# Optimization experiments

Hardware: AMD Instinct MI355X
Metric: run time of the kernel (lower is better)

## Reference

```python
import jax, jax.numpy as jnp
import numpy as np

NODE_CARDS = [119, 5, 12, 12, 10, 6, 6, 2, 2]
EDGE_CARDS = [5, 6, 2]
HIDDEN = 256
LAYERS = 5
N = 60000
E = 180000
G = 2048  # num graphs (fixed num_segments)
BN_EPS = 1e-5

_NODE_OFFS = np.concatenate([[0], np.cumsum(NODE_CARDS[:-1])]).astype(np.int32)
_EDGE_OFFS = np.concatenate([[0], np.cumsum(EDGE_CARDS[:-1])]).astype(np.int32)
_NODE_MAX = np.asarray(NODE_CARDS, np.int32) - 1
_EDGE_MAX = np.asarray(EDGE_CARDS, np.int32) - 1


def _cat_sum(x, table, maxs, offs):
    # x: [N, F] int; table: [sum(cards), H] -> [N, H]
    idx = jnp.clip(x, 0, maxs[None, :]) + offs[None, :]
    return table[idx].sum(axis=1)


def setup_inputs() -> dict:
    key = jax.random.key(0)
    ks = jax.random.split(key, 32)
    w = 0.0625  # ~ xavier for 256

    def nrm(k, shape, s=w):
        return jax.random.normal(k, shape, dtype=jnp.float32) * s

    inp = {
        'x': jax.random.randint(ks[0], (N, len(NODE_CARDS)), 0, 119, dtype=jnp.int32),
        'edge_index': jax.random.randint(ks[1], (2, E), 0, N, dtype=jnp.int32),
        'edge_attr': jax.random.randint(ks[2], (E, len(EDGE_CARDS)), 0, 6, dtype=jnp.int32),
        'batch': jnp.sort(jax.random.randint(ks[3], (N,), 0, G, dtype=jnp.int32)),
        # embeddings
        'node_emb': nrm(ks[4], (int(sum(NODE_CARDS)), HIDDEN), 0.1),
        'edge_emb': nrm(ks[5], (int(sum(EDGE_CARDS)), HIDDEN), 0.1),
        'vn_emb': nrm(ks[6], (1, HIDDEN), 0.1),
        # GINE conv: eps + 2-layer MLP per layer (stacked)
        'eps': jnp.zeros((LAYERS,), jnp.float32),
        'W1': nrm(ks[7], (LAYERS, HIDDEN, HIDDEN)),
        'b1': jnp.zeros((LAYERS, HIDDEN), jnp.float32),
        'W2': nrm(ks[8], (LAYERS, HIDDEN, HIDDEN)),
        'b2': jnp.zeros((LAYERS, HIDDEN), jnp.float32),
        # BatchNorm (eval mode: running stats)
        'bn_gamma': jnp.ones((LAYERS, HIDDEN), jnp.float32),
        'bn_beta': jnp.zeros((LAYERS, HIDDEN), jnp.float32),
        'bn_mean': nrm(ks[9], (LAYERS, HIDDEN), 0.02),
        'bn_var': jnp.ones((LAYERS, HIDDEN), jnp.float32),
        # virtual-node MLP per layer
        'vW1': nrm(ks[10], (LAYERS, HIDDEN, HIDDEN)),
        'vb1': jnp.zeros((LAYERS, HIDDEN), jnp.float32),
        'vW2': nrm(ks[11], (LAYERS, HIDDEN, HIDDEN)),
        'vb2': jnp.zeros((LAYERS, HIDDEN), jnp.float32),
        # head MLP (2 layers: hidden->hidden->1)
        'hW1': nrm(ks[12], (HIDDEN, HIDDEN)),
        'hb1': jnp.zeros((HIDDEN,), jnp.float32),
        'hW2': nrm(ks[13], (HIDDEN, 1)),
        'hb2': jnp.zeros((1,), jnp.float32),
    }
    return inp


def reference(x, edge_index, edge_attr, batch,
              node_emb, edge_emb, vn_emb, eps,
              W1, b1, W2, b2,
              bn_gamma, bn_beta, bn_mean, bn_var,
              vW1, vb1, vW2, vb2,
              hW1, hb1, hW2, hb2):
    node_maxs = jnp.asarray(_NODE_MAX)
    node_offs = jnp.asarray(_NODE_OFFS)
    edge_maxs = jnp.asarray(_EDGE_MAX)
    edge_offs = jnp.asarray(_EDGE_OFFS)

    h = _cat_sum(x, node_emb, node_maxs, node_offs)          # [N, H]
    ea = _cat_sum(edge_attr, edge_emb, edge_maxs, edge_offs)  # [E, H]
    src, dst = edge_index[0], edge_index[1]

    vn = jnp.broadcast_to(vn_emb[0], (G, HIDDEN))  # [G, H]

    def mean_pool(h_):
        s = jax.ops.segment_sum(h_, batch, num_segments=G)
        cnt = jax.ops.segment_sum(jnp.ones((h_.shape[0], 1), h_.dtype), batch, num_segments=G)
        return s / jnp.maximum(cnt, 1.0)

    for l in range(LAYERS):
        h = h + vn[batch]
        # GINEConv: msg = relu(x_src + edge_attr); agg scatter-add onto dst
        msg = jax.nn.relu(h[src] + ea)                        # [E, H]
        agg = jax.ops.segment_sum(msg, dst, num_segments=N)   # [N, H]
        z = (1.0 + eps[l]) * h + agg
        z = jax.nn.relu(z @ W1[l] + b1[l]) @ W2[l] + b2[l]
        # BatchNorm1d (eval, running stats)
        z = (z - bn_mean[l]) * (bn_gamma[l] / jnp.sqrt(bn_var[l] + BN_EPS)) + bn_beta[l]
        h = jax.nn.relu(z)
        # virtual-node update
        g = mean_pool(h)
        vn = vn + (jax.nn.relu(g @ vW1[l] + vb1[l]) @ vW2[l] + vb2[l])

    g = mean_pool(h)                                          # [G, H]
    logits = (jax.nn.relu(g @ hW1 + hb1) @ hW2 + hb2).reshape(-1)  # [G]
    return logits
```

## Files before the change

### kernel.cpp

```cpp
#include <hip/hip_runtime.h>

#define NN 60000
#define NE 180000
#define NG 2048
#define NL 5
#define CAP 32

typedef unsigned short u16;
typedef unsigned int u32;
typedef __bf16 bf16x8 __attribute__((ext_vector_type(8)));
typedef float f32x4 __attribute__((ext_vector_type(4)));

__device__ __forceinline__ u16 f2bf(float f) {
    u32 u = __builtin_bit_cast(u32, f);
    u += 0x7FFFu + ((u >> 16) & 1u);
    return (u16)(u >> 16);
}
__device__ __forceinline__ float bf2f(u16 s) {
    return __builtin_bit_cast(float, (u32)s << 16);
}
__device__ __forceinline__ float bflo(u32 w) {
    return __builtin_bit_cast(float, w << 16);
}
__device__ __forceinline__ float bfhi(u32 w) {
    return __builtin_bit_cast(float, w & 0xFFFF0000u);
}
__device__ __forceinline__ u32 pack2bf(float lo, float hi) {
    return (u32)f2bf(lo) | ((u32)f2bf(hi) << 16);
}
__device__ __forceinline__ void gload_lds16(const void* g, void* l) {
    __builtin_amdgcn_global_load_lds(
        (const __attribute__((address_space(1))) unsigned int*)g,
        (__attribute__((address_space(3))) unsigned int*)l, 16, 0, 0);
}
__device__ __forceinline__ int swz(int row, int col) {
    return (row << 9) + ((((col >> 3) ^ (row & 7))) << 4) + ((col & 7) << 1);
}

__constant__ int NODE_OFF[9]  = {0, 119, 124, 136, 148, 158, 164, 170, 172};
__constant__ int NODE_MAXC[9] = {118, 4, 11, 11, 9, 5, 5, 1, 1};

__global__ __launch_bounds__(256) void k_prep_weights(
    const float* __restrict__ W1, const float* __restrict__ W2,
    const float* __restrict__ vW1, const float* __restrict__ vW2,
    const float* __restrict__ hW1, u16* __restrict__ Wt)
{
    __shared__ float lt[64][65];
    int mat = blockIdx.x >> 4;
    int tile = blockIdx.x & 15;
    int tr = (tile >> 2) * 64;
    int tc = (tile & 3) * 64;
    const float* src;
    if (mat < 5)       src = W1 + (size_t)mat * 65536;
    else if (mat < 10) src = W2 + (size_t)(mat - 5) * 65536;
    else if (mat < 15) src = vW1 + (size_t)(mat - 10) * 65536;
    else if (mat < 20) src = vW2 + (size_t)(mat - 15) * 65536;
    else               src = hW1;
    int tid = threadIdx.x;
#pragma unroll
    for (int r = 0; r < 4; ++r) {
        int k = (tid >> 4) + r * 16;
        int c = (tid & 15) * 4;
        float4 v = *(const float4*)&src[(size_t)(tr + k) * 256 + tc + c];
        lt[k][c + 0] = v.x; lt[k][c + 1] = v.y;
        lt[k][c + 2] = v.z; lt[k][c + 3] = v.w;
    }
    __syncthreads();
#pragma unroll
    for (int r = 0; r < 4; ++r) {
        int n = (tid >> 4) + r * 16;
        int k = (tid & 15) * 4;
        ushort4 o;
        o.x = f2bf(lt[k + 0][n]); o.y = f2bf(lt[k + 1][n]);
        o.z = f2bf(lt[k + 2][n]); o.w = f2bf(lt[k + 3][n]);
        *(ushort4*)&Wt[(size_t)mat * 65536 + (size_t)(tc + n) * 256 + tr + k] = o;
    }
}

__global__ __launch_bounds__(256) void k_misc(
    const float* __restrict__ eemb, const int* __restrict__ batch,
    const float* __restrict__ vn_emb,
    u16* __restrict__ comb, int* __restrict__ starts,
    float* __restrict__ vn, u16* __restrict__ vnbf, float* __restrict__ gsum)
{
    int b = blockIdx.x;
    if (b < 2048) {
        int i = b * 256 + threadIdx.x;
        float v = vn_emb[i & 255];
        vn[i] = v;
        vnbf[i] = f2bf(v);
        gsum[i] = 0.f;
    } else if (b < 2108) {
        int r = b - 2048, c = threadIdx.x;
        int a0 = r / 12, a1 = (r % 12) / 2, a2 = r & 1;
        comb[r * 256 + c] = f2bf(eemb[a0 * 256 + c] + eemb[(5 + a1) * 256 + c] +
                                 eemb[(11 + a2) * 256 + c]);
    } else {
        int g = (b - 2108) * 256 + threadIdx.x;
        if (g > NG) return;
        int lo = 0, hi = NN;
        while (lo < hi) {
            int mid = (lo + hi) >> 1;
            if (batch[mid] < g) lo = mid + 1; else hi = mid;
        }
        starts[g] = lo;
    }
}

__global__ __launch_bounds__(256) void k_embed(const int* __restrict__ x,
                                               const float* __restrict__ node_emb,
                                               u16* __restrict__ hbf,
                                               int* __restrict__ deg)
{
    int i = blockIdx.x * 4 + (threadIdx.x >> 6);
    if (i >= NN) return;
    if ((threadIdx.x & 63) == 0) deg[i] = 0;
    int c = (threadIdx.x & 63) * 4;
    float4 s = make_float4(0.f, 0.f, 0.f, 0.f);
#pragma unroll
    for (int f = 0; f < 9; ++f) {
        int xv = x[i * 9 + f];
        xv = xv < 0 ? 0 : (xv > NODE_MAXC[f] ? NODE_MAXC[f] : xv);
        const float4 t = *(const float4*)&node_emb[(size_t)(NODE_OFF[f] + xv) * 256 + c];
        s.x += t.x; s.y += t.y; s.z += t.z; s.w += t.w;
    }
    ushort4 o;
    o.x = f2bf(s.x); o.y = f2bf(s.y); o.z = f2bf(s.z); o.w = f2bf(s.w);
    *(ushort4*)&hbf[(size_t)i * 256 + c] = o;
}

__global__ __launch_bounds__(256) void k_bucket(
    const int* __restrict__ src, const int* __restrict__ dst,
    const int* __restrict__ eattr, int* __restrict__ deg, u32* __restrict__ slots)
{
    int e = blockIdx.x * 256 + threadIdx.x;
    if (e >= NE) return;
    int a0 = eattr[e * 3 + 0]; a0 = a0 < 0 ? 0 : (a0 > 4 ? 4 : a0);
    int a1 = eattr[e * 3 + 1]; a1 = a1 < 0 ? 0 : (a1 > 5 ? 5 : a1);
    int a2 = eattr[e * 3 + 2]; a2 = a2 < 0 ? 0 : (a2 > 1 ? 1 : a2);
    u32 code = (u32)(a0 * 12 + a1 * 2 + a2);
    int d = dst[e];
    int p = atomicAdd(&deg[d], 1);
    if (p < CAP) slots[(size_t)d * CAP + p] = (u32)src[e] | (code << 17);
}

__global__ __launch_bounds__(256) void k_agg(
    const u16* __restrict__ hbf, const u16* __restrict__ vnbf,
    const int* __restrict__ batch, const u32* __restrict__ slots,
    const int* __restrict__ deg, const u16* __restrict__ comb,
    u16* __restrict__ Abf, const float* __restrict__ epsp)
{
    const int wid = threadIdx.x >> 6, lane = threadIdx.x & 63;
    const int half = lane >> 5, l32 = lane & 31;
    const int d = blockIdx.x * 8 + wid * 2 + half;
    const int c = l32 * 8;
    int nd = deg[d];
    nd = nd > CAP ? CAP : nd;

    const u32* sl = slots + (size_t)d * CAP;
    u32 sv_l = (l32 < nd) ? sl[l32] : 0u;
    int b_l = (l32 < nd) ? batch[sv_l & 0x1FFFFu] : 0;

    float acc[8] = {0.f, 0.f, 0.f, 0.f, 0.f, 0.f, 0.f, 0.f};
    for (int p = 0; p < nd; ++p) {
        int srcl = (lane & 32) | p;
        u32 sv = (u32)__shfl((int)sv_l, srcl);
        int b  = __shfl(b_l, srcl);
        int s  = (int)(sv & 0x1FFFFu);
        int code = (int)(sv >> 17);
        const uint4 hv = *(const uint4*)&hbf[(size_t)s * 256 + c];
        const uint4 vv = *(const uint4*)&vnbf[(size_t)b * 256 + c];
        const uint4 tv = *(const uint4*)&comb[(size_t)code * 256 + c];
        const u32* hw = (const u32*)&hv;
        const u32* vw = (const u32*)&vv;
        const u32* tw = (const u32*)&tv;
#pragma unroll
        for (int e = 0; e < 4; ++e) {
            acc[e * 2 + 0] += fmaxf(bflo(hw[e]) + bflo(vw[e]) + bflo(tw[e]), 0.f);
            acc[e * 2 + 1] += fmaxf(bfhi(hw[e]) + bfhi(vw[e]) + bfhi(tw[e]), 0.f);
        }
    }

    int bd = batch[d];
    float ep = 1.0f + *epsp;
    const uint4 hd = *(const uint4*)&hbf[(size_t)d * 256 + c];
    const uint4 vd = *(const uint4*)&vnbf[(size_t)bd * 256 + c];
    const u32* hw = (const u32*)&hd;
    const u32* vw = (const u32*)&vd;
    uint4 o;
    u32* op = (u32*)&o;
#pragma unroll
    for (int e = 0; e < 4; ++e) {
        float lo = (bflo(hw[e]) + bflo(vw[e])) * ep + acc[e * 2 + 0];
        float hi = (bfhi(hw[e]) + bfhi(vw[e])) * ep + acc[e * 2 + 1];
        op[e] = pack2bf(lo, hi);
    }
    *(uint4*)&Abf[(size_t)d * 256 + c] = o;
}

__device__ __forceinline__ void stageW(const u16* __restrict__ W, u16* Bl,
                                       int k0, int tid, int wid)
{
#pragma unroll
    for (int i = 0; i < 4; ++i) {
        int slot = i * 512 + tid;
        int row = slot >> 3, cch = slot & 7;
        int g = cch ^ (row & 7);
        gload_lds16((const char*)W + (size_t)row * 512 + (size_t)k0 * 2 + (g << 4),
                    (char*)Bl + ((i * 512 + wid * 64) << 4));
    }
}

__device__ __forceinline__ void gemm64(const u16* Tl, u16* Bl, const u16* __restrict__ W,
                                       f32x4 (&acc)[2][4], int wm, int wn,
                                       int lane, int tid, int wid)
{
    const int cl = lane & 15;
    for (int k0 = 0; k0 < 256; k0 += 64) {
        __syncthreads();
        stageW(W, Bl, k0, tid, wid);
        __syncthreads();
#pragma unroll
        for (int kw = 0; kw < 2; ++kw) {
            int q = kw * 4 + (lane >> 4);
            int qt = (k0 >> 3) + q;
            bf16x8 af[2], bfr[4];
#pragma unroll
            for (int t = 0; t < 2; ++t) {
                int ar = wm + t * 16 + cl;
                af[t] = __builtin_bit_cast(bf16x8,
                    *(const uint4*)((const char*)Tl + (ar << 9) + ((qt ^ (ar & 7)) << 4)));
            }
#pragma unroll
            for (int t = 0; t < 4; ++t) {
                int br = wn + t * 16 + cl;
                bfr[t] = __builtin_bit_cast(bf16x8,
                    *(const uint4*)((const char*)Bl + (br << 7) + ((q ^ (br & 7)) << 4)));
            }
#pragma unroll
            for (int i = 0; i < 2; ++i)
#pragma unroll
                for (int j = 0; j < 4; ++j)
                    acc[i][j] = __builtin_amdgcn_mfma_f32_16x16x32_bf16(af[i], bfr[j], acc[i][j], 0, 0, 0);
        }
    }
}

__device__ __forceinline__ void writeT(u16* Tl, const f32x4 (&acc)[2][4],
                                       const float* __restrict__ b1,
                                       int wm, int wn, int lane)
{
    const int cl = lane & 15, rg = lane >> 4;
#pragma unroll
    for (int j = 0; j < 4; ++j) {
        int col = wn + j * 16 + cl;
        float bv = b1[col];
#pragma unroll
        for (int i = 0; i < 2; ++i)
#pragma unroll
            for (int r = 0; r < 4; ++r) {
                int row = wm + i * 16 + rg * 4 + r;
                float v = fmaxf(acc[i][j][r] + bv, 0.f);
                *(u16*)((char*)Tl + swz(row, col)) = f2bf(v);
            }
    }
}

__global__ __launch_bounds__(512) void k_mlpP(
    const u16* __restrict__ Abf, u16* __restrict__ hnxt,
    const int* __restrict__ batch,
    const u16* __restrict__ W1t, const u16* __restrict__ W2t,
    const float* __restrict__ b1, const float* __restrict__ b2,
    const float* __restrict__ bng, const float* __restrict__ bnb,
    const float* __restrict__ bnm, const float* __restrict__ bnv,
    float* __restrict__ gsum)
{
    __shared__ __align__(16) u16 Bl[256 * 64];
    __shared__ __align__(16) u16 Tl[64 * 256];
    __shared__ int batchLds[64];
    const int m0 = blockIdx.x * 64;
    const int tid = threadIdx.x, lane = tid & 63, wid = tid >> 6;
    const int wm = (wid >> 2) * 32, wn = (wid & 3) * 64;
    const int cl = lane & 15, rg = lane >> 4;

    if (tid < 64) batchLds[tid] = (m0 + tid < NN) ? batch[m0 + tid] : -1;

#pragma unroll
    for (int i = 0; i < 4; ++i) {
        int slot = i * 512 + tid;
        int row = slot >> 5, cch = slot & 31;
        int g = cch ^ (row & 7);
        gload_lds16((const char*)Abf + (size_t)(m0 + row) * 512 + (g << 4),
                    (char*)Tl + ((i * 512 + wid * 64) << 4));
    }

    f32x4 acc1[2][4] = {};
    gemm64(Tl, Bl, W1t, acc1, wm, wn, lane, tid, wid);
    __syncthreads();
    writeT(Tl, acc1, b1, wm, wn, lane);

    f32x4 acc2[2][4] = {};
    gemm64(Tl, Bl, W2t, acc2, wm, wn, lane, tid, wid);
    __syncthreads();

#pragma unroll
    for (int j = 0; j < 4; ++j) {
        int gn = wn + j * 16 + cl;
        float bv = b2[gn];
        float sc = bng[gn] * rsqrtf(bnv[gn] + 1e-5f);
        float sh = bnb[gn] - bnm[gn] * sc;
        float s = 0.f;
        int gcur = -1;
#pragma unroll
        for (int i = 0; i < 2; ++i) {
#pragma unroll
            for (int r = 0; r < 4; ++r) {
                int row = wm + i * 16 + rg * 4 + r;
                int g = batchLds[row];
                float v = acc2[i][j][r] + bv;
                u16 hb = f2bf(fmaxf(v * sc + sh, 0.f));
                if (g >= 0) hnxt[(size_t)(m0 + row) * 256 + gn] = hb;
                if (g != gcur) {
                    if (gcur >= 0) atomicAdd(&gsum[(size_t)gcur * 256 + gn], s);
                    gcur = g; s = 0.f;
                }
                if (g >= 0) s += bf2f(hb);
            }
        }
        if (gcur >= 0) atomicAdd(&gsum[(size_t)gcur * 256 + gn], s);
    }
}

__global__ __launch_bounds__(512) void k_mlpR(
    const u16* __restrict__ Abf, u16* __restrict__ hnxt,
    const int* __restrict__ batch,
    const u16* __restrict__ W1t, const u16* __restrict__ W2t,
    const float* __restrict__ b1, const float* __restrict__ b2,
    const float* __restrict__ bng, const float* __restrict__ bnb,
    const float* __restrict__ bnm, const float* __restrict__ bnv,
    float* __restrict__ gsum)
{
    __shared__ __align__(16) u16 Wl[256 * 256];
    __shared__ __align__(16) u16 Tl[64 * 256];
    const int m0 = blockIdx.x * 64;
    const int tid = threadIdx.x, lane = tid & 63, wid = tid >> 6;
    const int wm = (wid >> 2) * 32, wn = (wid & 3) * 64;
    const int cl = lane & 15, rg = lane >> 4;

#pragma unroll
    for (int i = 0; i < 4; ++i) {
        int slot = i * 512 + tid;
        int row = slot >> 5, cch = slot & 31;
        int g = cch ^ (row & 7);
        gload_lds16((const char*)Abf + (size_t)(m0 + row) * 512 + (g << 4),
                    (char*)Tl + ((i * 512 + wid * 64) << 4));
    }
#pragma unroll
    for (int i = 0; i < 16; ++i) {
        int slot = i * 512 + tid;
        int row = slot >> 5, cch = slot & 31;
        int g = cch ^ (row & 7);
        gload_lds16((const char*)W1t + (size_t)row * 512 + (g << 4),
                    (char*)Wl + ((i * 512 + wid * 64) << 4));
    }
    __syncthreads();

    f32x4 acc1[2][4] = {};
#pragma unroll
    for (int p = 0; p < 8; ++p) {
        int ch = p * 4 + rg;
        bf16x8 af[2], bfr[4];
#pragma unroll
        for (int t = 0; t < 2; ++t) {
            int ar = wm + t * 16 + cl;
            af[t] = __builtin_bit_cast(bf16x8,
                *(const uint4*)((const char*)Tl + (ar << 9) + ((ch ^ (ar & 7)) << 4)));
        }
#pragma unroll
        for (int u = 0; u < 4; ++u) {
            int br = wn + u * 16 + cl;
            bfr[u] = __builtin_bit_cast(bf16x8,
                *(const uint4*)((const char*)Wl + (br << 9) + ((ch ^ (br & 7)) << 4)));
        }
#pragma unroll
        for (int t = 0; t < 2; ++t)
#pragma unroll
            for (int u = 0; u < 4; ++u)
                acc1[t][u] = __builtin_amdgcn_mfma_f32_16x16x32_bf16(af[t], bfr[u], acc1[t][u], 0, 0, 0);
    }
    __syncthreads();

    writeT(Tl, acc1, b1, wm, wn, lane);
#pragma unroll
    for (int i = 0; i < 16; ++i) {
        int slot = i * 512 + tid;
        int row = slot >> 5, cch = slot & 31;
        int g = cch ^ (row & 7);
        gload_lds16((const char*)W2t + (size_t)row * 512 + (g << 4),
                    (char*)Wl + ((i * 512 + wid * 64) << 4));
    }
    __syncthreads();

    f32x4 acc2[2][4] = {};
#pragma unroll
    for (int p = 0; p < 8; ++p) {
        int ch = p * 4 + rg;
        bf16x8 af[2], bfr[4];
#pragma unroll
        for (int t = 0; t < 2; ++t) {
            int ar = wm + t * 16 + cl;
            af[t] = __builtin_bit_cast(bf16x8,
                *(const uint4*)((const char*)Tl + (ar << 9) + ((ch ^ (ar & 7)) << 4)));
        }
#pragma unroll
        for (int u = 0; u < 4; ++u) {
            int br = wn + u * 16 + cl;
            bfr[u] = __builtin_bit_cast(bf16x8,
                *(const uint4*)((const char*)Wl + (br << 9) + ((ch ^ (br & 7)) << 4)));
        }
#pragma unroll
        for (int t = 0; t < 2; ++t)
#pragma unroll
            for (int u = 0; u < 4; ++u)
                acc2[t][u] = __builtin_amdgcn_mfma_f32_16x16x32_bf16(af[t], bfr[u], acc2[t][u], 0, 0, 0);
    }

#pragma unroll
    for (int j = 0; j < 4; ++j) {
        int gn = wn + j * 16 + cl;
        float bv = b2[gn];
        float sc = bng[gn] * rsqrtf(bnv[gn] + 1e-5f);
        float sh = bnb[gn] - bnm[gn] * sc;
        float s = 0.f;
        int gcur = -1;
#pragma unroll
        for (int i = 0; i < 2; ++i) {
#pragma unroll
            for (int r = 0; r < 4; ++r) {
                int row = wm + i * 16 + rg * 4 + r;
                int g = (m0 + row < NN) ? batch[m0 + row] : -1;
                float v = acc2[i][j][r] + bv;
                u16 hb = f2bf(fmaxf(v * sc + sh, 0.f));
                if (g >= 0) hnxt[(size_t)(m0 + row) * 256 + gn] = hb;
                if (g != gcur) {
                    if (gcur >= 0) atomicAdd(&gsum[(size_t)gcur * 256 + gn], s);
                    gcur = g; s = 0.f;
                }
                if (g >= 0) s += bf2f(hb);
            }
        }
        if (gcur >= 0) atomicAdd(&gsum[(size_t)gcur * 256 + gn], s);
    }
}

__global__ __launch_bounds__(512) void k_vnmlp(
    float* __restrict__ gsum, const int* __restrict__ starts,
    const u16* __restrict__ W1t, const u16* __restrict__ W2t,
    const float* __restrict__ b1, const float* __restrict__ b2,
    float* __restrict__ vn, u16* __restrict__ vnbf)
{
    __shared__ __align__(16) u16 Bl[256 * 64];
    __shared__ __align__(16) u16 Tl[64 * 256];
    const int m0 = blockIdx.x * 64;
    const int tid = threadIdx.x, lane = tid & 63, wid = tid >> 6;
    const int wm = (wid >> 2) * 32, wn = (wid & 3) * 64;
    const int cl = lane & 15, rg = lane >> 4;

    {
        const int c = lane * 4;
#pragma unroll
        for (int n = 0; n < 8; ++n) {
            int row = wid * 8 + n;
            int g = m0 + row;
            float4 sv = *(const float4*)&gsum[(size_t)g * 256 + c];
            *(float4*)&gsum[(size_t)g * 256 + c] = make_float4(0.f, 0.f, 0.f, 0.f);
            float cnt = (float)(starts[g + 1] - starts[g]);
            float inv = 1.0f / fmaxf(cnt, 1.0f);
            ushort4 o;
            o.x = f2bf(sv.x * inv); o.y = f2bf(sv.y * inv);
            o.z = f2bf(sv.z * inv); o.w = f2bf(sv.w * inv);
            *(ushort4*)((char*)Tl + swz(row, c)) = o;
        }
    }
    __syncthreads();

    f32x4 acc1[2][4] = {};
    gemm64(Tl, Bl, W1t, acc1, wm, wn, lane, tid, wid);
    __syncthreads();
    writeT(Tl, acc1, b1, wm, wn, lane);

    f32x4 acc2[2][4] = {};
    gemm64(Tl, Bl, W2t, acc2, wm, wn, lane, tid, wid);

#pragma unroll
    for (int j = 0; j < 4; ++j) {
        int gn = wn + j * 16 + cl;
        float bv = b2[gn];
#pragma unroll
        for (int i = 0; i < 2; ++i) {
#pragma unroll
            for (int r = 0; r < 4; ++r) {
                int gm = m0 + wm + i * 16 + rg * 4 + r;
                size_t idx = (size_t)gm * 256 + gn;
                float nv = vn[idx] + acc2[i][j][r] + bv;
                vn[idx] = nv;
                vnbf[idx] = f2bf(nv);
            }
        }
    }
}

__global__ __launch_bounds__(512) void k_headf(
    const float* __restrict__ gsum, const int* __restrict__ starts,
    const u16* __restrict__ W1t, const float* __restrict__ b1,
    const float* __restrict__ hW2, const float* __restrict__ hb2,
    float* __restrict__ out)
{
    __shared__ __align__(16) u16 Bl[256 * 64];
    __shared__ __align__(16) u16 Tl[64 * 256];
    const int m0 = blockIdx.x * 64;
    const int tid = threadIdx.x, lane = tid & 63, wid = tid >> 6;
    const int wm = (wid >> 2) * 32, wn = (wid & 3) * 64;

    {
        const int c = lane * 4;
#pragma unroll
        for (int n = 0; n < 8; ++n) {
            int row = wid * 8 + n;
            int g = m0 + row;
            float4 sv = *(const float4*)&gsum[(size_t)g * 256 + c];
            float cnt = (float)(starts[g + 1] - starts[g]);
            float inv = 1.0f / fmaxf(cnt, 1.0f);
            ushort4 o;
            o.x = f2bf(sv.x * inv); o.y = f2bf(sv.y * inv);
            o.z = f2bf(sv.z * inv); o.w = f2bf(sv.w * inv);
            *(ushort4*)((char*)Tl + swz(row, c)) = o;
        }
    }
    __syncthreads();

    f32x4 acc1[2][4] = {};
    gemm64(Tl, Bl, W1t, acc1, wm, wn, lane, tid, wid);
    __syncthreads();
    writeT(Tl, acc1, b1, wm, wn, lane);
    __syncthreads();

    int row = tid >> 3, oct = tid & 7;
    float s = 0.f;
#pragma unroll
    for (int c = 0; c < 32; ++c) {
        int col = oct * 32 + c;
        s += bf2f(*(const u16*)((const char*)Tl + swz(row, col))) * hW2[col];
    }
    s += __shfl_down(s, 4);
    s += __shfl_down(s, 2);
    s += __shfl_down(s, 1);
    if (oct == 0) out[m0 + row] = s + hb2[0];
}

extern "C" void kernel_launch(void* const* d_in, const int* in_sizes, int n_in,
                              void* d_out, int out_size, void* d_ws, size_t ws_size,
                              hipStream_t stream)
{
    const int*   x        = (const int*)d_in[0];
    const int*   ei       = (const int*)d_in[1];
    const int*   eattr    = (const int*)d_in[2];
    const int*   batch    = (const int*)d_in[3];
    const float* node_emb = (const float*)d_in[4];
    const float* edge_emb = (const float*)d_in[5];
    const float* vn_emb   = (const float*)d_in[6];
    const float* eps      = (const float*)d_in[7];
    const float* W1       = (const float*)d_in[8];
    const float* b1       = (const float*)d_in[9];
    const float* W2       = (const float*)d_in[10];
    const float* b2       = (const float*)d_in[11];
    const float* bng      = (const float*)d_in[12];
    const float* bnb      = (const float*)d_in[13];
    const float* bnm      = (const float*)d_in[14];
    const float* bnv      = (const float*)d_in[15];
    const float* vW1      = (const float*)d_in[16];
    const float* vb1      = (const float*)d_in[17];
    const float* vW2      = (const float*)d_in[18];
    const float* vb2      = (const float*)d_in[19];
    const float* hW1      = (const float*)d_in[20];
    const float* hb1      = (const float*)d_in[21];
    const float* hW2      = (const float*)d_in[22];
    const float* hb2      = (const float*)d_in[23];
    float* out = (float*)d_out;

    char* ws = (char*)d_ws;
    size_t off = 0;
    auto alloc = [&](size_t b) {
        char* p = ws + off;
        off = (off + b + 255) & ~(size_t)255;
        return p;
    };
    u16*   hbf0 = (u16*)alloc((size_t)NN * 256 * 2);
    u16*   hbf1 = (u16*)alloc((size_t)NN * 256 * 2);
    u16*   Abf  = (u16*)alloc((size_t)NN * 256 * 2 + 65536);
    float* vn   = (float*)alloc((size_t)NG * 256 * 4);
    u16*   vnbf = (u16*)alloc((size_t)NG * 256 * 2);
    float* gsum = (float*)alloc((size_t)NG * 256 * 4);
    u16*   Wt   = (u16*)alloc((size_t)21 * 65536 * 2);
    int*   starts = (int*)alloc((size_t)(NG + 1) * 4);
    u16*   comb = (u16*)alloc((size_t)60 * 256 * 2);
    int*   deg  = (int*)alloc((size_t)NN * 4);
    u32*   slots = (u32*)alloc((size_t)NN * CAP * 4);

    const int* srcI = ei;
    const int* dstI = ei + NE;

    k_prep_weights<<<21 * 16, 256, 0, stream>>>(W1, W2, vW1, vW2, hW1, Wt);
    k_misc<<<2117, 256, 0, stream>>>(edge_emb, batch, vn_emb, comb, starts, vn, vnbf, gsum);
    k_embed<<<NN / 4, 256, 0, stream>>>(x, node_emb, hbf0, deg);
    k_bucket<<<(NE + 255) / 256, 256, 0, stream>>>(srcI, dstI, eattr, deg, slots);

    const int GBIG = (NN + 63) / 64;
    const int GSM  = NG / 64;

    u16* hcur = hbf0;
    u16* hnxt = hbf1;
    for (int l = 0; l < NL; ++l) {
        k_agg<<<NN / 8, 256, 0, stream>>>(hcur, vnbf, batch, slots, deg, comb, Abf, eps + l);
        const u16* w1p = Wt + (size_t)(0 + l) * 65536;
        const u16* w2p = Wt + (size_t)(5 + l) * 65536;
        if (l == 1 || l == 3) {
            k_mlpR<<<GBIG, 512, 0, stream>>>(Abf, hnxt, batch, w1p, w2p,
                                             b1 + l * 256, b2 + l * 256,
                                             bng + l * 256, bnb + l * 256,
                                             bnm + l * 256, bnv + l * 256, gsum);
        } else {
            k_mlpP<<<GBIG, 512, 0, stream>>>(Abf, hnxt, batch, w1p, w2p,
                                             b1 + l * 256, b2 + l * 256,
                                             bng + l * 256, bnb + l * 256,
                                             bnm + l * 256, bnv + l * 256, gsum);
        }
        if (l < NL - 1) {
            k_vnmlp<<<GSM, 512, 0, stream>>>(gsum, starts,
                                             Wt + (size_t)(10 + l) * 65536,
                                             Wt + (size_t)(15 + l) * 65536,
                                             vb1 + l * 256, vb2 + l * 256,
                                             vn, vnbf);
        }
        u16* t = hcur; hcur = hnxt; hnxt = t;
    }
    k_headf<<<GSM, 512, 0, stream>>>(gsum, starts, Wt + (size_t)20 * 65536,
                                     hb1, hW2, hb2, out);
}
```

Measured before the change: 601.9 us.

## Replace full-weight-in-LDS MLP with 32-row tiles streaming K-chunks of weights

Replaces the k_mlpR variant, which staged the whole 256x256 weight matrix (128KB) in LDS per 64-row block, with k_mlpS, which handles 32 rows per block and streams 64-wide K slices of W1/W2 through a 32KB LDS buffer. The goal is lower LDS use, which allows more resident blocks and twice the grid size for better occupancy. In exchange it adds per-chunk syncs and reloads the weights more often per row. The new kernel runs on layers 0, 2 and 4 instead of the old kernel's layers 1 and 3, and it reads batch ids once into LDS.

Measured after the change: 545.9 us. 9.3% less time.

```diff
diff --git a/kernel.cpp b/kernel.cpp
--- a/kernel.cpp
+++ b/kernel.cpp
@@ -331,7 +331,7 @@
     }
 }
 
-__global__ __launch_bounds__(512) void k_mlpR(
+__global__ __launch_bounds__(512) void k_mlpS(
     const u16* __restrict__ Abf, u16* __restrict__ hnxt,
     const int* __restrict__ batch,
     const u16* __restrict__ W1t, const u16* __restrict__ W2t,
@@ -340,93 +340,102 @@
     const float* __restrict__ bnm, const float* __restrict__ bnv,
     float* __restrict__ gsum)
 {
-    __shared__ __align__(16) u16 Wl[256 * 256];
-    __shared__ __align__(16) u16 Tl[64 * 256];
-    const int m0 = blockIdx.x * 64;
+    __shared__ __align__(16) u16 Bl[256 * 64];
+    __shared__ __align__(16) u16 Tl[32 * 256];
+    __shared__ int batchLds[32];
+    const int m0 = blockIdx.x * 32;
     const int tid = threadIdx.x, lane = tid & 63, wid = tid >> 6;
-    const int wm = (wid >> 2) * 32, wn = (wid & 3) * 64;
+    const int wn = wid * 32;
     const int cl = lane & 15, rg = lane >> 4;
 
-#pragma unroll
-    for (int i = 0; i < 4; ++i) {
+    if (tid < 32) batchLds[tid] = batch[m0 + tid];
+
+#pragma unroll
+    for (int i = 0; i < 2; ++i) {
         int slot = i * 512 + tid;
         int row = slot >> 5, cch = slot & 31;
         int g = cch ^ (row & 7);
         gload_lds16((const char*)Abf + (size_t)(m0 + row) * 512 + (g << 4),
                     (char*)Tl + ((i * 512 + wid * 64) << 4));
     }
-#pragma unroll
-    for (int i = 0; i < 16; ++i) {
-        int slot = i * 512 + tid;
-        int row = slot >> 5, cch = slot & 31;
-        int g = cch ^ (row & 7);
-        gload_lds16((const char*)W1t + (size_t)row * 512 + (g << 4),
-                    (char*)Wl + ((i * 512 + wid * 64) << 4));
-    }
-    __syncthreads();
-
-    f32x4 acc1[2][4] = {};
-#pragma unroll
-    for (int p = 0; p < 8; ++p) {
-        int ch = p * 4 + rg;
-        bf16x8 af[2], bfr[4];
-#pragma unroll
-        for (int t = 0; t < 2; ++t) {
-            int ar = wm + t * 16 + cl;
-            af[t] = __builtin_bit_cast(bf16x8,
-                *(const uint4*)((const char*)Tl + (ar << 9) + ((ch ^ (ar & 7)) << 4)));
-        }
-#pragma unroll
-        for (int u = 0; u < 4; ++u) {
-            int br = wn + u * 16 + cl;
-            bfr[u] = __builtin_bit_cast(bf16x8,
-                *(const uint4*)((const char*)Wl + (br << 9) + ((ch ^ (br & 7)) << 4)));
-        }
-#pragma unroll
-        for (int t = 0; t < 2; ++t)
-#pragma unroll
-            for (int u = 0; u < 4; ++u)
-                acc1[t][u] = __builtin_amdgcn_mfma_f32_16x16x32_bf16(af[t], bfr[u], acc1[t][u], 0, 0, 0);
-    }
-    __syncthreads();
-
-    writeT(Tl, acc1, b1, wm, wn, lane);
-#pragma unroll
-    for (int i = 0; i < 16; ++i) {
-        int slot = i * 512 + tid;
-        int row = slot >> 5, cch = slot & 31;
-        int g = cch ^ (row & 7);
-        gload_lds16((const char*)W2t + (size_t)row * 512 + (g << 4),
-                    (char*)Wl + ((i * 512 + wid * 64) << 4));
-    }
-    __syncthreads();
-
-    f32x4 acc2[2][4] = {};
-#pragma unroll
-    for (int p = 0; p < 8; ++p) {
-        int ch = p * 4 + rg;
-        bf16x8 af[2], bfr[4];
-#pragma unroll
-        for (int t = 0; t < 2; ++t) {
-            int ar = wm + t * 16 + cl;
-            af[t] = __builtin_bit_cast(bf16x8,
-                *(const uint4*)((const char*)Tl + (ar << 9) + ((ch ^ (ar & 7)) << 4)));
-        }
-#pragma unroll
-        for (int u = 0; u < 4; ++u) {
-            int br = wn + u * 16 + cl;
-            bfr[u] = __builtin_bit_cast(bf16x8,
-                *(const uint4*)((const char*)Wl + (br << 9) + ((ch ^ (br & 7)) << 4)));
-        }
-#pragma unroll
-        for (int t = 0; t < 2; ++t)
-#pragma unroll
-            for (int u = 0; u < 4; ++u)
-                acc2[t][u] = __builtin_amdgcn_mfma_f32_16x16x32_bf16(af[t], bfr[u], acc2[t][u], 0, 0, 0);
-    }
-
-#pragma unroll
-    for (int j = 0; j < 4; ++j) {
+
+    f32x4 acc1[2][2] = {};
+    for (int k0 = 0; k0 < 256; k0 += 64) {
+        __syncthreads();
+        stageW(W1t, Bl, k0, tid, wid);
+        __syncthreads();
+#pragma unroll
+        for (int kw = 0; kw < 2; ++kw) {
+            int q = kw * 4 + rg;
+            int qt = (k0 >> 3) + q;
+            bf16x8 af[2], bfr[2];
+#pragma unroll
+            for (int t = 0; t < 2; ++t) {
+                int ar = t * 16 + cl;
+                af[t] = __builtin_bit_cast(bf16x8,
+                    *(const uint4*)((const char*)Tl + (ar << 9) + ((qt ^ (ar & 7)) << 4)));
+            }
+#pragma unroll
+            for (int u = 0; u < 2; ++u) {
+                int br = wn + u * 16 + cl;
+                bfr[u] = __builtin_bit_cast(bf16x8,
+                    *(const uint4*)((const char*)Bl + (br << 7) + ((q ^ (br & 7)) << 4)));
+            }
+#pragma unroll
+            for (int t = 0; t < 2; ++t)
+#pragma unroll
+                for (int u = 0; u < 2; ++u)
+                    acc1[t][u] = __builtin_amdgcn_mfma_f32_16x16x32_bf16(af[t], bfr[u], acc1[t][u], 0, 0, 0);
+        }
+    }
+    __syncthreads();
+
+#pragma unroll
+    for (int j = 0; j < 2; ++j) {
+        int col = wn + j * 16 + cl;
+        float bv = b1[col];
+#pragma unroll
+        for (int i = 0; i < 2; ++i)
+#pragma unroll
+            for (int r = 0; r < 4; ++r) {
+                int row = i * 16 + rg * 4 + r;
+                float v = fmaxf(acc1[i][j][r] + bv, 0.f);
+                *(u16*)((char*)Tl + swz(row, col)) = f2bf(v);
+            }
+    }
+
+    f32x4 acc2[2][2] = {};
+    for (int k0 = 0; k0 < 256; k0 += 64) {
+        __syncthreads();
+        stageW(W2t, Bl, k0, tid, wid);
+        __syncthreads();
+#pragma unroll
+        for (int kw = 0; kw < 2; ++kw) {
+            int q = kw * 4 + rg;
+            int qt = (k0 >> 3) + q;
+            bf16x8 af[2], bfr[2];
+#pragma unroll
+            for (int t = 0; t < 2; ++t) {
+                int ar = t * 16 + cl;
+                af[t] = __builtin_bit_cast(bf16x8,
+                    *(const uint4*)((const char*)Tl + (ar << 9) + ((qt ^ (ar & 7)) << 4)));
+            }
+#pragma unroll
+            for (int u = 0; u < 2; ++u) {
+                int br = wn + u * 16 + cl;
+                bfr[u] = __builtin_bit_cast(bf16x8,
+                    *(const uint4*)((const char*)Bl + (br << 7) + ((q ^ (br & 7)) << 4)));
+            }
+#pragma unroll
+            for (int t = 0; t < 2; ++t)
+#pragma unroll
+                for (int u = 0; u < 2; ++u)
+                    acc2[t][u] = __builtin_amdgcn_mfma_f32_16x16x32_bf16(af[t], bfr[u], acc2[t][u], 0, 0, 0);
+        }
+    }
+
+#pragma unroll
+    for (int j = 0; j < 2; ++j) {
         int gn = wn + j * 16 + cl;
         float bv = b2[gn];
         float sc = bng[gn] * rsqrtf(bnv[gn] + 1e-5f);
@@ -437,16 +446,16 @@
         for (int i = 0; i < 2; ++i) {
 #pragma unroll
             for (int r = 0; r < 4; ++r) {
-                int row = wm + i * 16 + rg * 4 + r;
-                int g = (m0 + row < NN) ? batch[m0 + row] : -1;
+                int row = i * 16 + rg * 4 + r;
+                int g = batchLds[row];
                 float v = acc2[i][j][r] + bv;
                 u16 hb = f2bf(fmaxf(v * sc + sh, 0.f));
-                if (g >= 0) hnxt[(size_t)(m0 + row) * 256 + gn] = hb;
+                hnxt[(size_t)(m0 + row) * 256 + gn] = hb;
                 if (g != gcur) {
                     if (gcur >= 0) atomicAdd(&gsum[(size_t)gcur * 256 + gn], s);
                     gcur = g; s = 0.f;
                 }
-                if (g >= 0) s += bf2f(hb);
+                s += bf2f(hb);
             }
         }
         if (gcur >= 0) atomicAdd(&gsum[(size_t)gcur * 256 + gn], s);
@@ -616,6 +625,7 @@
     k_bucket<<<(NE + 255) / 256, 256, 0, stream>>>(srcI, dstI, eattr, deg, slots);
 
     const int GBIG = (NN + 63) / 64;
+    const int GS32 = NN / 32;
     const int GSM  = NG / 64;
 
     u16* hcur = hbf0;
@@ -624,8 +634,8 @@
         k_agg<<<NN / 8, 256, 0, stream>>>(hcur, vnbf, batch, slots, deg, comb, Abf, eps + l);
         const u16* w1p = Wt + (size_t)(0 + l) * 65536;
         const u16* w2p = Wt + (size_t)(5 + l) * 65536;
-        if (l == 1 || l == 3) {
-            k_mlpR<<<GBIG, 512, 0, stream>>>(Abf, hnxt, batch, w1p, w2p,
+        if (l == 0 || l == 2 || l == 4) {
+            k_mlpS<<<GS32, 512, 0, stream>>>(Abf, hnxt, batch, w1p, w2p,
                                              b1 + l * 256, b2 + l * 256,
                                              bng + l * 256, bnb + l * 256,
                                              bnm + l * 256, bnv + l * 256, gsum);
```
